# Kernel optimization log

Measured on AMD Instinct MI355X. Metric: run time of the kernel, lower is better.

The kernel has to match this reference:

```python
import jax, jax.numpy as jnp
import numpy as np

D = 768
H = 12
HD = D // H
NEG = -10000.0
EPS = 1e-12


def setup_inputs() -> dict:
    key = jax.random.key(0)
    ks = jax.random.split(key, 8)
    B, S = 4, 1024
    xavier = lambda k: jax.random.normal(k, (D, D), dtype=jnp.float32) * np.sqrt(2.0 / (D + D))
    return {
        "embeddings": jax.random.normal(ks[0], (B, S, D), dtype=jnp.float32),
        "padding_mask": jnp.ones((B, S), dtype=jnp.float32),
        "wq_w": xavier(ks[1]), "wq_b": jnp.zeros((D,), jnp.float32),
        "wk_w": xavier(ks[2]), "wk_b": jnp.zeros((D,), jnp.float32),
        "wv_w": xavier(ks[3]), "wv_b": jnp.zeros((D,), jnp.float32),
        "wo_w": xavier(ks[4]), "wo_b": jnp.zeros((D,), jnp.float32),
        "ln_g": jnp.ones((D,), jnp.float32), "ln_b": jnp.zeros((D,), jnp.float32),
    }


def reference(embeddings, padding_mask, wq_w, wq_b, wk_w, wk_b, wv_w, wv_b, wo_w, wo_b, ln_g, ln_b):
    B, S, _ = embeddings.shape
    # QKV projections (torch Linear: x @ W^T + b), split heads -> [B,H,S,HD]
    split = lambda t: t.reshape(B, S, H, HD).transpose(0, 2, 1, 3)
    q = split(embeddings @ wq_w.T + wq_b)
    k = split(embeddings @ wk_w.T + wk_b)
    v = split(embeddings @ wv_w.T + wv_b)
    # NOTE: original scales by sqrt(embedding_dim), not sqrt(per-head dim)
    attn = jnp.einsum("bhqd,bhkd->bhqk", q, k) / jnp.sqrt(jnp.float32(D))
    # additive padding mask, then causal masked_fill (set, not add)
    attn = attn + ((1.0 - padding_mask)[:, None, None, :] * NEG)
    causal = jnp.tril(jnp.ones((S, S), dtype=jnp.float32))
    attn = jnp.where(causal[None, None] == 0, NEG, attn)
    attn_probs = jax.nn.softmax(attn, axis=-1)  # dropout is identity at inference
    ctx = jnp.einsum("bhqk,bhkd->bhqd", attn_probs, v)
    ctx = ctx.transpose(0, 2, 1, 3).reshape(B, S, D)
    attn_out = ctx @ wo_w.T + wo_b  # keep_prob = 1.0 -> no rescale
    # residual + LayerNorm(eps=1e-12)
    x = attn_out + embeddings
    mu = jnp.mean(x, axis=-1, keepdims=True)
    var = jnp.mean((x - mu) ** 2, axis=-1, keepdims=True)
    normed = (x - mu) * jax.lax.rsqrt(var + EPS) * ln_g + ln_b
    return (normed, attn_probs)
```

## Files before the change

kernel.cpp:

```cpp
#include <hip/hip_runtime.h>
#include <hip/hip_bf16.h>

typedef __bf16 bf16x8 __attribute__((ext_vector_type(8)));
typedef float  f32x4  __attribute__((ext_vector_type(4)));

#define NEGC (-10000.0f)

static __device__ __forceinline__ void glds16(const __bf16* src, __bf16* dst) {
    __builtin_amdgcn_global_load_lds((const __attribute__((address_space(1))) unsigned int*)src,
                                     (__attribute__((address_space(3))) unsigned int*)dst, 16, 0, 0);
}

__global__ __launch_bounds__(256) void cvt_all(
    const float* __restrict__ emb, const float* __restrict__ wq, const float* __restrict__ wk,
    const float* __restrict__ wv, const float* __restrict__ wo,
    __bf16* __restrict__ Xb, __bf16* __restrict__ Wall)
{
    int blk = blockIdx.x;
    const float* src; __bf16* dst; int i;
    if (blk < 1536) {
        src = emb; dst = Xb; i = blk * 256 + threadIdx.x;
    } else {
        int b2 = blk - 1536;
        int which = b2 / 288;
        src = which == 0 ? wq : which == 1 ? wk : which == 2 ? wv : wo;
        dst = Wall + (size_t)which * 589824;
        i = (b2 - which * 288) * 256 + threadIdx.x;
    }
    f32x4 a = *(const f32x4*)(src + (size_t)i * 8);
    f32x4 b = *(const f32x4*)(src + (size_t)i * 8 + 4);
    bf16x8 o;
    o[0] = (__bf16)a[0]; o[1] = (__bf16)a[1]; o[2] = (__bf16)a[2]; o[3] = (__bf16)a[3];
    o[4] = (__bf16)b[0]; o[5] = (__bf16)b[1]; o[6] = (__bf16)b[2]; o[7] = (__bf16)b[3];
    *(bf16x8*)(dst + (size_t)i * 8) = o;
}

template<int MODE>
__global__ __launch_bounds__(256) void gemm128(
    const __bf16* __restrict__ A, const __bf16* __restrict__ Bw,
    const float* __restrict__ b0, const float* __restrict__ b1, const float* __restrict__ b2,
    __bf16* __restrict__ O0, __bf16* __restrict__ O1, __bf16* __restrict__ O2,
    const float* __restrict__ res, float* __restrict__ Yout)
{
    __shared__ __align__(16) __bf16 As[128 * 64];
    __shared__ __align__(16) __bf16 Bs[128 * 64];
    const int K = 768;
    const int NT = (MODE == 0) ? 18 : 6;
    int wgid = blockIdx.x;
    int xcd = wgid & 7;
    int t = wgid >> 3;
    int m0 = (xcd * 4 + t / NT) * 128;
    int n0 = (t % NT) * 128;

    int tid = threadIdx.x;
    int l = tid & 63, w = tid >> 6;
    int lo = l & 15, hi = l >> 4;
    int wr = w >> 1, wc = w & 1;

    f32x4 acc[4][4] = {};

    int srow = tid >> 3;
    int scb  = (tid & 7) ^ (srow & 7);
    const __bf16* gA = A + (size_t)(m0 + srow) * K + scb * 8;
    const __bf16* gB = Bw + (size_t)(n0 + srow) * K + scb * 8;
    __bf16* lA = As + tid * 8;
    __bf16* lB = Bs + tid * 8;

    for (int k0 = 0; k0 < K; k0 += 64) {
        if (k0) __syncthreads();
#pragma unroll
        for (int p = 0; p < 4; p++) {
            glds16(gA + (size_t)p * 32 * K + k0, lA + p * 2048);
            glds16(gB + (size_t)p * 32 * K + k0, lB + p * 2048);
        }
        __syncthreads();

#pragma unroll
        for (int kk = 0; kk < 2; kk++) {
            bf16x8 af[4], bfr[4];
#pragma unroll
            for (int mi = 0; mi < 4; mi++)
                af[mi] = *(const bf16x8*)(As + (wr * 64 + mi * 16 + lo) * 64 + (((kk * 4 + hi) ^ (lo & 7)) * 8));
#pragma unroll
            for (int ni = 0; ni < 4; ni++)
                bfr[ni] = *(const bf16x8*)(Bs + (wc * 64 + ni * 16 + lo) * 64 + (((kk * 4 + hi) ^ (lo & 7)) * 8));
#pragma unroll
            for (int mi = 0; mi < 4; mi++)
#pragma unroll
                for (int ni = 0; ni < 4; ni++)
                    acc[mi][ni] = __builtin_amdgcn_mfma_f32_16x16x32_bf16(af[mi], bfr[ni], acc[mi][ni], 0, 0, 0);
        }
    }

    if constexpr (MODE == 0) {
        int which = n0 / 768;
        const float* bias = which == 0 ? b0 : (which == 1 ? b1 : b2);
        __bf16* O = which == 0 ? O0 : (which == 1 ? O1 : O2);
        int nbase = n0 - which * 768;
#pragma unroll
        for (int mi = 0; mi < 4; mi++)
#pragma unroll
            for (int ni = 0; ni < 4; ni++) {
                int within = nbase + wc * 64 + ni * 16 + lo;
                float bv = bias[within];
                int h = within >> 6, d = within & 63;
#pragma unroll
                for (int i = 0; i < 4; i++) {
                    int m = m0 + wr * 64 + mi * 16 + hi * 4 + i;
                    int bb = m >> 10, s = m & 1023;
                    O[(size_t)((bb * 12 + h) * 1024 + s) * 64 + d] = (__bf16)(acc[mi][ni][i] + bv);
                }
            }
    } else {
#pragma unroll
        for (int mi = 0; mi < 4; mi++)
#pragma unroll
            for (int ni = 0; ni < 4; ni++) {
                int n = n0 + wc * 64 + ni * 16 + lo;
                float bv = b0[n];
#pragma unroll
                for (int i = 0; i < 4; i++) {
                    int m = m0 + wr * 64 + mi * 16 + hi * 4 + i;
                    size_t idx = (size_t)m * 768 + n;
                    Yout[idx] = acc[mi][ni][i] + bv + res[idx];
                }
            }
    }
}

__global__ __launch_bounds__(256) void attn_kernel(
    const __bf16* __restrict__ Q, const __bf16* __restrict__ K, const __bf16* __restrict__ V,
    const float* __restrict__ pmask, float* __restrict__ Pout, __bf16* __restrict__ ctx)
{
    int wgid = blockIdx.x;
    int xcd = wgid & 7;
    int t = wgid >> 3;
    int bh = xcd * 6 + (t % 6);
    int y = t / 6;
    int b = bh / 12, h = bh - b * 12;
    int q0 = y * 64;
    int tid = threadIdx.x, l = tid & 63, w = tid >> 6;
    int lo = l & 15, hi = l >> 4;
    int qw = q0 + w * 16;

    const __bf16* Qh = Q + (size_t)bh * 65536;
    const __bf16* Kh = K + (size_t)bh * 65536;
    const __bf16* Vh = V + (size_t)bh * 65536;
    float* Ph = Pout + (size_t)bh * 1048576;
    const float* pm = pmask + b * 1024;

    __shared__ __align__(16) __bf16 Ks[2][64][64];
    __shared__ __align__(16) __bf16 vt[2][64][72];
    __shared__ __align__(16) __bf16 plds[4][16][72];

    const float scale = 0.036084391824351615f;

    bf16x8 qf0 = *(const bf16x8*)(Qh + (size_t)(qw + lo) * 64 + hi * 8);
    bf16x8 qf1 = *(const bf16x8*)(Qh + (size_t)(qw + lo) * 64 + 32 + hi * 8);

    int srow = tid >> 3;
    int scb  = (tid & 7) ^ (srow & 7);
    __bf16* ldst0 = &Ks[0][0][0] + tid * 8;

#define STAGE_K(buf, kt)  do {                                             \
        glds16(Kh + (size_t)((kt) * 64 + srow) * 64 + scb * 8,             \
               ldst0 + (buf) * 4096);                                      \
        glds16(Kh + (size_t)((kt) * 64 + 32 + srow) * 64 + scb * 8,        \
               ldst0 + (buf) * 4096 + 2048);                               \
    } while (0)

#define KFRAG(buf, kn, dh) \
    (*(const bf16x8*)(&Ks[buf][(kn) * 16 + lo][(((dh) * 4 + hi) ^ (lo & 7)) * 8]))

#define WAITV(n)  asm volatile("s_waitcnt vmcnt(" #n ")" ::: "memory")
#define WAITL     asm volatile("s_waitcnt lgkmcnt(0)" ::: "memory")
#define BAR       __builtin_amdgcn_s_barrier()

    float lsum[4] = {};
    STAGE_K(0, 0);
    for (int kt = 0; kt <= y; kt++) {
        int cur = kt & 1;
        if (kt < y) { STAGE_K(cur ^ 1, kt + 1); WAITV(2); }
        else        { WAITV(0); }
        BAR;
        int k0 = kt * 64;
        float pad[4];
#pragma unroll
        for (int kn = 0; kn < 4; kn++) pad[kn] = (1.0f - pm[k0 + kn * 16 + lo]) * NEGC;
        f32x4 s[4] = {};
        __builtin_amdgcn_s_setprio(1);
#pragma unroll
        for (int kn = 0; kn < 4; kn++) {
            s[kn] = __builtin_amdgcn_mfma_f32_16x16x32_bf16(qf0, KFRAG(cur, kn, 0), s[kn], 0, 0, 0);
            s[kn] = __builtin_amdgcn_mfma_f32_16x16x32_bf16(qf1, KFRAG(cur, kn, 1), s[kn], 0, 0, 0);
        }
        __builtin_amdgcn_s_setprio(0);
#pragma unroll
        for (int kn = 0; kn < 4; kn++) {
            int c = k0 + kn * 16 + lo;
#pragma unroll
            for (int i = 0; i < 4; i++) {
                int r = qw + hi * 4 + i;
                float a = s[kn][i] * scale + pad[kn];
                if (c > r) a = NEGC;
                lsum[i] += __expf(a);
            }
        }
        WAITL; BAR;
    }

    float invl[4];
#pragma unroll
    for (int i = 0; i < 4; i++) {
        float s = lsum[i];
        s += __shfl_xor(s, 1);
        s += __shfl_xor(s, 2);
        s += __shfl_xor(s, 4);
        s += __shfl_xor(s, 8);
        invl[i] = 1.0f / s;
    }

    int vrow = tid >> 2, vcol = (tid & 3) * 16;
    bf16x8 va, vb;
    {
        STAGE_K(0, 0);
        const __bf16* vp = Vh + (size_t)vrow * 64 + vcol;
        va = *(const bf16x8*)vp; vb = *(const bf16x8*)(vp + 8);
#pragma unroll
        for (int j = 0; j < 8; j++) vt[0][vcol + j][vrow] = va[j];
#pragma unroll
        for (int j = 0; j < 8; j++) vt[0][vcol + 8 + j][vrow] = vb[j];
        if (y > 0) {
            const __bf16* vp1 = Vh + (size_t)(64 + vrow) * 64 + vcol;
            va = *(const bf16x8*)vp1; vb = *(const bf16x8*)(vp1 + 8);
        }
        __syncthreads();
    }

    f32x4 cacc[4] = {};
    for (int kt = 0; kt <= y; kt++) {
        int cur = kt & 1;
        if (kt < y) STAGE_K(cur ^ 1, kt + 1);
        WAITV(16);
        BAR;
        int k0 = kt * 64;
        float pad[4];
#pragma unroll
        for (int kn = 0; kn < 4; kn++) pad[kn] = (1.0f - pm[k0 + kn * 16 + lo]) * NEGC;
        f32x4 s[4] = {};
        __builtin_amdgcn_s_setprio(1);
#pragma unroll
        for (int kn = 0; kn < 4; kn++) {
            s[kn] = __builtin_amdgcn_mfma_f32_16x16x32_bf16(qf0, KFRAG(cur, kn, 0), s[kn], 0, 0, 0);
            s[kn] = __builtin_amdgcn_mfma_f32_16x16x32_bf16(qf1, KFRAG(cur, kn, 1), s[kn], 0, 0, 0);
        }
        __builtin_amdgcn_s_setprio(0);
#pragma unroll
        for (int kn = 0; kn < 4; kn++) {
            int c = k0 + kn * 16 + lo;
#pragma unroll
            for (int i = 0; i < 4; i++) {
                int r = qw + hi * 4 + i;
                float a = s[kn][i] * scale + pad[kn];
                if (c > r) a = NEGC;
                float p = __expf(a) * invl[i];
                Ph[(size_t)r * 1024 + c] = p;
                plds[w][hi * 4 + i][kn * 16 + lo] = (__bf16)p;
            }
        }
        __builtin_amdgcn_s_setprio(1);
#pragma unroll
        for (int ks = 0; ks < 2; ks++) {
            bf16x8 pf = *(const bf16x8*)(&plds[w][lo][ks * 32 + hi * 8]);
#pragma unroll
            for (int dt = 0; dt < 4; dt++) {
                bf16x8 vf = *(const bf16x8*)(&vt[cur][dt * 16 + lo][ks * 32 + hi * 8]);
                cacc[dt] = __builtin_amdgcn_mfma_f32_16x16x32_bf16(pf, vf, cacc[dt], 0, 0, 0);
            }
        }
        __builtin_amdgcn_s_setprio(0);
        if (kt < y) {
#pragma unroll
            for (int j = 0; j < 8; j++) vt[cur ^ 1][vcol + j][vrow] = va[j];
#pragma unroll
            for (int j = 0; j < 8; j++) vt[cur ^ 1][vcol + 8 + j][vrow] = vb[j];
            if (kt + 1 < y) {
                const __bf16* vp = Vh + (size_t)((kt + 2) * 64 + vrow) * 64 + vcol;
                va = *(const bf16x8*)vp; vb = *(const bf16x8*)(vp + 8);
            }
        }
        WAITL; BAR;
    }

#pragma unroll
    for (int dt = 0; dt < 4; dt++) {
#pragma unroll
        for (int i = 0; i < 4; i++) {
            int m = b * 1024 + qw + hi * 4 + i;
            int n = h * 64 + dt * 16 + lo;
            ctx[(size_t)m * 768 + n] = (__bf16)cacc[dt][i];
        }
    }

    for (int c = (y + 1) * 64 + lo * 4; c < 1024; c += 64) {
#pragma unroll
        for (int i = 0; i < 4; i++) {
            f32x4 z = {};
            *(f32x4*)(Ph + (size_t)(qw + hi * 4 + i) * 1024 + c) = z;
        }
    }
#undef STAGE_K
#undef KFRAG
#undef WAITV
#undef WAITL
#undef BAR
}

__global__ __launch_bounds__(256) void ln_kernel(
    const float* __restrict__ Y, const float* __restrict__ g, const float* __restrict__ bta,
    float* __restrict__ out)
{
    int row = blockIdx.x * 4 + (threadIdx.x >> 6);
    int l = threadIdx.x & 63;
    const float* yr = Y + (size_t)row * 768;
    f32x4 v0 = *(const f32x4*)(yr + l * 4);
    f32x4 v1 = *(const f32x4*)(yr + 256 + l * 4);
    f32x4 v2 = *(const f32x4*)(yr + 512 + l * 4);
    float s = v0[0] + v0[1] + v0[2] + v0[3] + v1[0] + v1[1] + v1[2] + v1[3]
            + v2[0] + v2[1] + v2[2] + v2[3];
#pragma unroll
    for (int m = 1; m < 64; m <<= 1) s += __shfl_xor(s, m);
    float mu = s * (1.0f / 768.0f);
    float ss = 0.0f;
#pragma unroll
    for (int j = 0; j < 4; j++) {
        float d0 = v0[j] - mu, d1 = v1[j] - mu, d2 = v2[j] - mu;
        ss += d0 * d0 + d1 * d1 + d2 * d2;
    }
#pragma unroll
    for (int m = 1; m < 64; m <<= 1) ss += __shfl_xor(ss, m);
    float r = rsqrtf(ss * (1.0f / 768.0f) + 1e-12f);
    float* orow = out + (size_t)row * 768;
#pragma unroll
    for (int c = 0; c < 3; c++) {
        f32x4 v = (c == 0) ? v0 : ((c == 1) ? v1 : v2);
        int col = c * 256 + l * 4;
        f32x4 gg = *(const f32x4*)(g + col);
        f32x4 bb = *(const f32x4*)(bta + col);
        f32x4 o;
#pragma unroll
        for (int j = 0; j < 4; j++) o[j] = (v[j] - mu) * r * gg[j] + bb[j];
        *(f32x4*)(orow + col) = o;
    }
}

extern "C" void kernel_launch(void* const* d_in, const int* in_sizes, int n_in,
                              void* d_out, int out_size, void* d_ws, size_t ws_size,
                              hipStream_t stream)
{
    const float* emb   = (const float*)d_in[0];
    const float* pmask = (const float*)d_in[1];
    const float* wq = (const float*)d_in[2];  const float* bq = (const float*)d_in[3];
    const float* wk = (const float*)d_in[4];  const float* bk = (const float*)d_in[5];
    const float* wv = (const float*)d_in[6];  const float* bv = (const float*)d_in[7];
    const float* wo = (const float*)d_in[8];  const float* bo = (const float*)d_in[9];
    const float* lng = (const float*)d_in[10]; const float* lnb = (const float*)d_in[11];

    __bf16* Xb   = (__bf16*)d_ws;
    __bf16* Wall = Xb + 4096 * 768;
    __bf16* Qb   = Wall + 4 * 589824;
    __bf16* Kb   = Qb + 3145728;
    __bf16* Vb   = Kb + 3145728;
    __bf16* Cb   = Vb + 3145728;
    float*  Yf   = (float*)(Cb + 3145728);

    float* normed = (float*)d_out;
    float* probs  = normed + (size_t)4096 * 768;

    cvt_all<<<2688, 256, 0, stream>>>(emb, wq, wk, wv, wo, Xb, Wall);

    gemm128<0><<<576, 256, 0, stream>>>(Xb, Wall, bq, bk, bv, Qb, Kb, Vb, nullptr, nullptr);
    attn_kernel<<<768, 256, 0, stream>>>(Qb, Kb, Vb, pmask, probs, Cb);
    gemm128<1><<<192, 256, 0, stream>>>(Cb, Wall + 3 * 589824, bo, nullptr, nullptr,
                                        nullptr, nullptr, nullptr, emb, Yf);
    ln_kernel<<<1024, 256, 0, stream>>>(Yf, lng, lnb, normed);
}
```

Baseline: 117.9 us.

## Enlarge attention query tile to 128 rows with 512-thread blocks

Each attention workgroup now covers 128 query rows with 8 waves instead of 64 rows with 4 waves, launching half as many workgroups. Each K and V tile staged in LDS is reused by twice as many queries, and the staging loads are spread over 512 threads with one load each. The cost is that waves for the lower 64 rows also process the diagonal tile their upper half needs, doing masked work that contributes nothing. The smaller grid also gives coarser load balance across the triangular causal workload.

Measured after the change: 125.8 us. +6.7%, slower.

```diff
diff --git a/kernel.cpp b/kernel.cpp
--- a/kernel.cpp
+++ b/kernel.cpp
@@ -128,7 +128,7 @@
     }
 }
 
-__global__ __launch_bounds__(256) void attn_kernel(
+__global__ __launch_bounds__(512) void attn_kernel(
     const __bf16* __restrict__ Q, const __bf16* __restrict__ K, const __bf16* __restrict__ V,
     const float* __restrict__ pmask, float* __restrict__ Pout, __bf16* __restrict__ ctx)
 {
@@ -137,8 +137,9 @@
     int t = wgid >> 3;
     int bh = xcd * 6 + (t % 6);
     int y = t / 6;
+    int KTB = 2 * y + 1;
     int b = bh / 12, h = bh - b * 12;
-    int q0 = y * 64;
+    int q0 = y * 128;
     int tid = threadIdx.x, l = tid & 63, w = tid >> 6;
     int lo = l & 15, hi = l >> 4;
     int qw = q0 + w * 16;
@@ -151,7 +152,7 @@
 
     __shared__ __align__(16) __bf16 Ks[2][64][64];
     __shared__ __align__(16) __bf16 vt[2][64][72];
-    __shared__ __align__(16) __bf16 plds[4][16][72];
+    __shared__ __align__(16) __bf16 plds[8][16][72];
 
     const float scale = 0.036084391824351615f;
 
@@ -162,12 +163,8 @@
     int scb  = (tid & 7) ^ (srow & 7);
     __bf16* ldst0 = &Ks[0][0][0] + tid * 8;
 
-#define STAGE_K(buf, kt)  do {                                             \
-        glds16(Kh + (size_t)((kt) * 64 + srow) * 64 + scb * 8,             \
-               ldst0 + (buf) * 4096);                                      \
-        glds16(Kh + (size_t)((kt) * 64 + 32 + srow) * 64 + scb * 8,        \
-               ldst0 + (buf) * 4096 + 2048);                               \
-    } while (0)
+#define STAGE_K(buf, kt) \
+    glds16(Kh + (size_t)((kt) * 64 + srow) * 64 + scb * 8, ldst0 + (buf) * 4096)
 
 #define KFRAG(buf, kn, dh) \
     (*(const bf16x8*)(&Ks[buf][(kn) * 16 + lo][(((dh) * 4 + hi) ^ (lo & 7)) * 8]))
@@ -178,10 +175,10 @@
 
     float lsum[4] = {};
     STAGE_K(0, 0);
-    for (int kt = 0; kt <= y; kt++) {
+    for (int kt = 0; kt <= KTB; kt++) {
         int cur = kt & 1;
-        if (kt < y) { STAGE_K(cur ^ 1, kt + 1); WAITV(2); }
-        else        { WAITV(0); }
+        if (kt < KTB) { STAGE_K(cur ^ 1, kt + 1); WAITV(1); }
+        else          { WAITV(0); }
         BAR;
         int k0 = kt * 64;
         float pad[4];
@@ -220,27 +217,22 @@
         invl[i] = 1.0f / s;
     }
 
-    int vrow = tid >> 2, vcol = (tid & 3) * 16;
-    bf16x8 va, vb;
+    int vrow = tid >> 3, vcol = (tid & 7) * 8;
+    bf16x8 va;
     {
         STAGE_K(0, 0);
         const __bf16* vp = Vh + (size_t)vrow * 64 + vcol;
-        va = *(const bf16x8*)vp; vb = *(const bf16x8*)(vp + 8);
-#pragma unroll
-        for (int j = 0; j < 8; j++) vt[0][vcol + j][vrow] = va[j];
-#pragma unroll
-        for (int j = 0; j < 8; j++) vt[0][vcol + 8 + j][vrow] = vb[j];
-        if (y > 0) {
-            const __bf16* vp1 = Vh + (size_t)(64 + vrow) * 64 + vcol;
-            va = *(const bf16x8*)vp1; vb = *(const bf16x8*)(vp1 + 8);
-        }
+        bf16x8 v0 = *(const bf16x8*)vp;
+#pragma unroll
+        for (int j = 0; j < 8; j++) vt[0][vcol + j][vrow] = v0[j];
+        va = *(const bf16x8*)(Vh + (size_t)(64 + vrow) * 64 + vcol);
         __syncthreads();
     }
 
     f32x4 cacc[4] = {};
-    for (int kt = 0; kt <= y; kt++) {
+    for (int kt = 0; kt <= KTB; kt++) {
         int cur = kt & 1;
-        if (kt < y) STAGE_K(cur ^ 1, kt + 1);
+        if (kt < KTB) STAGE_K(cur ^ 1, kt + 1);
         WAITV(16);
         BAR;
         int k0 = kt * 64;
@@ -279,15 +271,11 @@
             }
         }
         __builtin_amdgcn_s_setprio(0);
-        if (kt < y) {
+        if (kt < KTB) {
 #pragma unroll
             for (int j = 0; j < 8; j++) vt[cur ^ 1][vcol + j][vrow] = va[j];
-#pragma unroll
-            for (int j = 0; j < 8; j++) vt[cur ^ 1][vcol + 8 + j][vrow] = vb[j];
-            if (kt + 1 < y) {
-                const __bf16* vp = Vh + (size_t)((kt + 2) * 64 + vrow) * 64 + vcol;
-                va = *(const bf16x8*)vp; vb = *(const bf16x8*)(vp + 8);
-            }
+            if (kt + 1 < KTB)
+                va = *(const bf16x8*)(Vh + (size_t)((kt + 2) * 64 + vrow) * 64 + vcol);
         }
         WAITL; BAR;
     }
@@ -302,7 +290,7 @@
         }
     }
 
-    for (int c = (y + 1) * 64 + lo * 4; c < 1024; c += 64) {
+    for (int c = (KTB + 1) * 64 + lo * 4; c < 1024; c += 64) {
 #pragma unroll
         for (int i = 0; i < 4; i++) {
             f32x4 z = {};
@@ -380,7 +368,7 @@
     cvt_all<<<2688, 256, 0, stream>>>(emb, wq, wk, wv, wo, Xb, Wall);
 
     gemm128<0><<<576, 256, 0, stream>>>(Xb, Wall, bq, bk, bv, Qb, Kb, Vb, nullptr, nullptr);
-    attn_kernel<<<768, 256, 0, stream>>>(Qb, Kb, Vb, pmask, probs, Cb);
+    attn_kernel<<<384, 512, 0, stream>>>(Qb, Kb, Vb, pmask, probs, Cb);
     gemm128<1><<<192, 256, 0, stream>>>(Cb, Wall + 3 * 589824, bo, nullptr, nullptr,
                                         nullptr, nullptr, nullptr, emb, Yf);
     ln_kernel<<<1024, 256, 0, stream>>>(Yf, lng, lnb, normed);
```
